# Kernel tuning notes

Measured on AMD Instinct MI355X. Metric: run time of the kernel, lower is better.

The kernel has to match this reference:

```python
import jax, jax.numpy as jnp
import numpy as np

DIM = 64
H = 4
POS_DIM = 4
NUM_IDS = 16
B = 2048
N = 64


def setup_inputs() -> dict:
    key = jax.random.key(0)
    ks = jax.random.split(key, 16)
    d8 = DIM // 8
    stdv = 1.0 / np.sqrt(DIM * DIM)
    inp = {
        "x": jax.random.normal(ks[0], (B, N, DIM), jnp.float32),
        "pos": jax.random.normal(ks[1], (B, N, POS_DIM), jnp.float32),
        "strength": jax.random.normal(ks[2], (512,), jnp.float32),
        "embed_id1": 3,
        # weights stored [in, out] (torch Linear weight transposed)
        "Wq": jax.random.normal(ks[3], (DIM, DIM), jnp.float32) * 0.05,
        "Wk": jax.random.normal(ks[4], (DIM, DIM), jnp.float32) * 0.05,
        "pos_W1": jax.random.normal(ks[5], (POS_DIM, POS_DIM), jnp.float32) * 0.3,
        "pos_b1": jnp.zeros((POS_DIM,), jnp.float32),
        "pos_W2": jax.random.normal(ks[6], (POS_DIM, d8), jnp.float32) * 0.3,
        "pos_b2": jnp.zeros((d8,), jnp.float32),
        "head_W": jax.random.normal(ks[7], (d8, H), jnp.float32) * 0.3,
        "head_b": jnp.zeros((H,), jnp.float32),
        "gate": jnp.ones((H,), jnp.float32),
        "embeds": jax.random.uniform(ks[8], (NUM_IDS, DIM * DIM), jnp.float32, -stdv, stdv),
        "out_W": jax.random.normal(ks[9], (DIM, DIM), jnp.float32) * 0.05,
        "out_b": jnp.zeros((DIM,), jnp.float32),
        "str_W": jax.random.normal(ks[10], (512, 64), jnp.float32) * 0.04,
        "str_b": jnp.zeros((64,), jnp.float32),
    }
    return inp


def reference(x, pos, strength, embed_id1, Wq, Wk, pos_W1, pos_b1, pos_W2, pos_b2,
              head_W, head_b, gate, embeds, out_W, out_b, str_W, str_b):
    Bb, Nn, dim = x.shape
    h = gate.shape[0]
    dh = dim // h

    # strength projection, added to dynamic-weight V
    s64 = strength @ str_W + str_b                       # [dim]
    E = embeds[embed_id1].reshape(dim, dim)              # per-sample V weight
    v = x @ E.T + s64                                    # F.linear(x, E) + strength
    v = v.reshape(Bb, Nn, h, dh).transpose(0, 2, 1, 3)   # [B,H,N,dh]

    # QK attention
    q = (x @ Wq).reshape(Bb, Nn, h, dh).transpose(0, 2, 1, 3)
    k = (x @ Wk).reshape(Bb, Nn, h, dh).transpose(0, 2, 1, 3)
    attn = jax.nn.softmax(jnp.einsum('bhqd,bhkd->bhqk', q, k) / np.sqrt(dh), axis=-1)

    # pairwise relative-position attention
    p = jax.nn.relu(pos @ pos_W1 + pos_b1) @ pos_W2 + pos_b2          # [B,N,dim//8]
    diff = p[:, :, None, :] - p[:, None, :, :]                        # [B,N,N,dim//8]
    pos_logits = jnp.einsum('bqkf,fh->bhqk', diff, head_W) + head_b[None, :, None, None]
    pos_attn = jax.nn.softmax(pos_logits, axis=-1)

    # sigmoid-gated mixing + renormalization
    g = jax.nn.sigmoid(gate)[None, :, None, None]
    attn = (1.0 - g) * attn + g * pos_attn
    attn = attn / jnp.sum(attn, axis=-1, keepdims=True)

    out = jnp.einsum('bhqk,bhkd->bhqd', attn, v)
    out = out.transpose(0, 2, 1, 3).reshape(Bb, Nn, dim)
    return out @ out_W + out_b
```

## Files before the change

kernel.cpp:

```cpp
#include <hip/hip_runtime.h>

typedef unsigned short u16;
typedef unsigned int u32;
typedef short bf8 __attribute__((ext_vector_type(8)));
typedef float f4v __attribute__((ext_vector_type(4)));
typedef float f16v __attribute__((ext_vector_type(16)));

#define STR 72

__device__ __forceinline__ u32 f2bf(float f){
    union{float f;u32 i;}c; c.f=f; u32 i=c.i;
    return (i + 0x7FFFu + ((i>>16)&1u)) >> 16;
}

__device__ __forceinline__ void stage_row16(const float* __restrict__ g, short* __restrict__ dst,
                                            int n, int c0){
    const float4* p = (const float4*)(g + n*64 + c0);
    float4 a=p[0], b=p[1], c=p[2], d=p[3];
    uint4 o0, o1;
    o0.x = f2bf(a.x)|(f2bf(a.y)<<16); o0.y = f2bf(a.z)|(f2bf(a.w)<<16);
    o0.z = f2bf(b.x)|(f2bf(b.y)<<16); o0.w = f2bf(b.z)|(f2bf(b.w)<<16);
    o1.x = f2bf(c.x)|(f2bf(c.y)<<16); o1.y = f2bf(c.z)|(f2bf(c.w)<<16);
    o1.z = f2bf(d.x)|(f2bf(d.y)<<16); o1.w = f2bf(d.z)|(f2bf(d.w)<<16);
    *(uint4*)&dst[n*STR + c0]     = o0;
    *(uint4*)&dst[n*STR + c0 + 8] = o1;
}

__device__ __forceinline__ void copy8k(const u16* __restrict__ src, short* __restrict__ dst, int t){
    const int r = t >> 2, cs = (t & 3) << 4;
    const uint4* s = (const uint4*)(src + r*64 + cs);
    uint4 a = s[0], b = s[1];
    *(uint4*)&dst[r*STR + cs]     = a;
    *(uint4*)&dst[r*STR + cs + 8] = b;
}

__device__ __forceinline__ void mmlin(const short* __restrict__ X, const short* __restrict__ Wt,
                                      int w, int l15, int quad, f4v c[4]){
    bf8 a0 = *(const bf8*)&X[(16*w + l15)*STR + quad*8];
    bf8 a1 = *(const bf8*)&X[(16*w + l15)*STR + 32 + quad*8];
    #pragma unroll
    for (int nt=0; nt<4; ++nt){
        bf8 b0 = *(const bf8*)&Wt[(16*nt + l15)*STR + quad*8];
        bf8 b1 = *(const bf8*)&Wt[(16*nt + l15)*STR + 32 + quad*8];
        c[nt] = __builtin_amdgcn_mfma_f32_16x16x32_bf16(a0, b0, c[nt], 0,0,0);
        c[nt] = __builtin_amdgcn_mfma_f32_16x16x32_bf16(a1, b1, c[nt], 0,0,0);
    }
}

__global__ __launch_bounds__(256) void pre_kernel(
    const float* __restrict__ pos, const float* __restrict__ strength,
    const int* __restrict__ embed_id,
    const float* __restrict__ Wq, const float* __restrict__ Wk,
    const float* __restrict__ pW1, const float* __restrict__ pb1,
    const float* __restrict__ pW2, const float* __restrict__ pb2,
    const float* __restrict__ hW, const float* __restrict__ embeds,
    const float* __restrict__ oW, const float* __restrict__ sW,
    const float* __restrict__ sb,
    float* __restrict__ ws_s64, float* __restrict__ ws_pat,
    u16* __restrict__ ws_wq, u16* __restrict__ ws_wk,
    u16* __restrict__ ws_ow, u16* __restrict__ ws_e, int B)
{
    const int blk = blockIdx.x;
    const int t = threadIdx.x;

    if (blk < B) {
        __shared__ float t_l[4][64];
        if (t < 64) {
            float pv[4], h1[4], p8[8];
            const float* gp = pos + ((size_t)blk*64 + t)*4;
            #pragma unroll
            for (int i = 0; i < 4; ++i) pv[i] = gp[i];
            #pragma unroll
            for (int j = 0; j < 4; ++j){
                float a = pb1[j];
                #pragma unroll
                for (int i = 0; i < 4; ++i) a = fmaf(pv[i], pW1[i*4+j], a);
                h1[j] = fmaxf(a, 0.f);
            }
            #pragma unroll
            for (int f = 0; f < 8; ++f){
                float a = pb2[f];
                #pragma unroll
                for (int j = 0; j < 4; ++j) a = fmaf(h1[j], pW2[j*8+f], a);
                p8[f] = a;
            }
            #pragma unroll
            for (int h = 0; h < 4; ++h){
                float a = 0.f;
                #pragma unroll
                for (int f = 0; f < 8; ++f) a = fmaf(p8[f], hW[f*4+h], a);
                t_l[h][t] = a;
            }
        }
        __syncthreads();
        const int h = t >> 6, k = t & 63;
        float v0 = -t_l[h][k];
        float m = v0;
        #pragma unroll
        for (int off = 32; off; off >>= 1) m = fmaxf(m, __shfl_xor(m, off));
        float e = __expf(v0 - m);
        float ssum = e;
        #pragma unroll
        for (int off = 32; off; off >>= 1) ssum += __shfl_xor(ssum, off);
        ws_pat[((size_t)blk*4 + h)*64 + k] = e / ssum;
        return;
    }

    const int j = blk - B;
    if (j < 3) {
        const float* W = (j==0) ? Wq : (j==1) ? Wk : oW;
        u16* dst = (j==0) ? ws_wq : (j==1) ? ws_wk : ws_ow;
        const int kp = t >> 3, ng = t & 7;
        const float4* r0 = (const float4*)(W + (2*kp  )*64 + 8*ng);
        const float4* r1 = (const float4*)(W + (2*kp+1)*64 + 8*ng);
        float4 a0=r0[0], a1=r0[1], b0=r1[0], b1=r1[1];
        float lo[8]={a0.x,a0.y,a0.z,a0.w,a1.x,a1.y,a1.z,a1.w};
        float hi[8]={b0.x,b0.y,b0.z,b0.w,b1.x,b1.y,b1.z,b1.w};
        #pragma unroll
        for (int i=0;i<8;++i)
            *(u32*)&dst[(8*ng+i)*64 + 2*kp] = f2bf(lo[i]) | (f2bf(hi[i])<<16);
    } else {
        __shared__ float sp[4][64];
        {
            const int n = t >> 2, c0 = (t & 3) << 4;
            const float4* p = (const float4*)(embeds + (size_t)(*embed_id)*4096 + n*64 + c0);
            float4 a=p[0], b=p[1], c=p[2], d=p[3];
            uint4 o0, o1;
            o0.x = f2bf(a.x)|(f2bf(a.y)<<16); o0.y = f2bf(a.z)|(f2bf(a.w)<<16);
            o0.z = f2bf(b.x)|(f2bf(b.y)<<16); o0.w = f2bf(b.z)|(f2bf(b.w)<<16);
            o1.x = f2bf(c.x)|(f2bf(c.y)<<16); o1.y = f2bf(c.z)|(f2bf(c.w)<<16);
            o1.z = f2bf(d.x)|(f2bf(d.y)<<16); o1.w = f2bf(d.z)|(f2bf(d.w)<<16);
            *(uint4*)&ws_e[n*64 + c0]     = o0;
            *(uint4*)&ws_e[n*64 + c0 + 8] = o1;
        }
        {
            const int d = t & 63, part = t >> 6;
            const float* wp = sW + part*128*64 + d;
            const float* s  = strength + part*128;
            float acc = 0.f;
            #pragma unroll 8
            for (int i = 0; i < 128; ++i) acc = fmaf(s[i], wp[i*64], acc);
            sp[part][d] = acc;
        }
        __syncthreads();
        if (t < 64) ws_s64[t] = sp[0][t] + sp[1][t] + sp[2][t] + sp[3][t] + sb[t];
    }
}

__global__ __launch_bounds__(256, 2) void attn_main_kernel(
    const float* __restrict__ x, const float* __restrict__ gate, const float* __restrict__ ob,
    const float* __restrict__ ws_s64, const float* __restrict__ ws_pat,
    const u16* __restrict__ ws_wq, const u16* __restrict__ ws_wk,
    const u16* __restrict__ ws_ow, const u16* __restrict__ ws_e,
    float* __restrict__ out)
{
    __shared__ short B0[64*STR];
    __shared__ short B1[64*STR];
    __shared__ short B2[64*STR];
    __shared__ short B3[64*STR];
    __shared__ short VT[64*STR];
    __shared__ short PX[64*STR];

    const int t    = threadIdx.x;
    const int b    = blockIdx.x;
    const int lane = t & 63;
    const int w    = t >> 6;
    const int l15  = lane & 15;
    const int l31  = lane & 31;
    const int l5   = lane >> 5;
    const int quad = lane >> 4;
    const int n    = t >> 2;
    const int c0   = (t & 3) << 4;

    stage_row16(x + (size_t)b*4096, B0, n, c0);
    copy8k(ws_wq, B1, t);
    copy8k(ws_wk, VT, t);

    uint4 eA, eB, owA, owB;
    {
        const int r = t >> 2, cs = (t & 3) << 4;
        const uint4* se = (const uint4*)(ws_e + r*64 + cs);
        eA = se[0]; eB = se[1];
        const uint4* so = (const uint4*)(ws_ow + r*64 + cs);
        owA = so[0]; owB = so[1];
    }
    float svv[4];
    #pragma unroll
    for (int nt=0;nt<4;++nt) svv[nt] = ws_s64[16*nt + l15];
    float g = 1.f/(1.f + __expf(-gate[w]));
    float obv[4];
    #pragma unroll
    for (int nt=0;nt<4;++nt) obv[nt] = ob[16*nt + l15];
    __syncthreads();

    {
        f4v cq[4], ck[4];
        #pragma unroll
        for (int nt=0;nt<4;++nt){
            cq[nt][0]=0.f;cq[nt][1]=0.f;cq[nt][2]=0.f;cq[nt][3]=0.f;
            ck[nt][0]=0.f;ck[nt][1]=0.f;ck[nt][2]=0.f;ck[nt][3]=0.f;
        }
        mmlin(B0, B1, w, l15, quad, cq);
        mmlin(B0, VT, w, l15, quad, ck);
        __syncthreads();
        #pragma unroll
        for (int nt=0;nt<4;++nt)
            #pragma unroll
            for (int r=0;r<4;++r){
                B2[(16*w + quad*4 + r)*STR + 16*nt + l15] = (short)f2bf(0.25f*cq[nt][r]);
                B3[(16*w + quad*4 + r)*STR + 16*nt + l15] = (short)f2bf(ck[nt][r]);
            }
        const int r = t >> 2, cs = (t & 3) << 4;
        *(uint4*)&B1[r*STR + cs]     = eA;
        *(uint4*)&B1[r*STR + cs + 8] = eB;
    }
    __syncthreads();

    {
        f4v c[4];
        #pragma unroll
        for (int nt=0;nt<4;++nt){ c[nt][0]=0.f;c[nt][1]=0.f;c[nt][2]=0.f;c[nt][3]=0.f; }
        mmlin(B0, B1, w, l15, quad, c);
        __syncthreads();
        #pragma unroll
        for (int nt=0;nt<4;++nt){
            float sv = svv[nt];
            uint2 pk;
            pk.x = f2bf(c[nt][0]+sv) | (f2bf(c[nt][1]+sv)<<16);
            pk.y = f2bf(c[nt][2]+sv) | (f2bf(c[nt][3]+sv)<<16);
            *(uint2*)&VT[(16*nt + l15)*STR + 16*w + quad*4] = pk;
        }
        const int r = t >> 2, cs = (t & 3) << 4;
        *(uint4*)&B1[r*STR + cs]     = owA;
        *(uint4*)&B1[r*STR + cs + 8] = owB;
    }
    __syncthreads();

    f16v S[2][2];
    {
        bf8 ka0 = *(const bf8*)&B3[(     l31)*STR + 16*w + 8*l5];
        bf8 ka1 = *(const bf8*)&B3[(32 + l31)*STR + 16*w + 8*l5];
        bf8 qb0 = *(const bf8*)&B2[(     l31)*STR + 16*w + 8*l5];
        bf8 qb1 = *(const bf8*)&B2[(32 + l31)*STR + 16*w + 8*l5];
        #pragma unroll
        for (int mt=0;mt<2;++mt)
            #pragma unroll
            for (int nt=0;nt<2;++nt)
                #pragma unroll
                for (int i=0;i<16;++i) S[mt][nt][i] = 0.f;
        S[0][0] = __builtin_amdgcn_mfma_f32_32x32x16_bf16(ka0, qb0, S[0][0], 0,0,0);
        S[0][1] = __builtin_amdgcn_mfma_f32_32x32x16_bf16(ka0, qb1, S[0][1], 0,0,0);
        S[1][0] = __builtin_amdgcn_mfma_f32_32x32x16_bf16(ka1, qb0, S[1][0], 0,0,0);
        S[1][1] = __builtin_amdgcn_mfma_f32_32x32x16_bf16(ka1, qb1, S[1][1], 0,0,0);
    }
    float ep[32];
    {
        const float* pp = ws_pat + ((size_t)b*4 + w)*64;
        #pragma unroll
        for (int mt=0;mt<2;++mt)
            #pragma unroll
            for (int rg=0;rg<4;++rg){
                float4 tv = *(const float4*)&pp[32*mt + 8*rg + 4*l5];
                ep[mt*16+rg*4+0] = g*tv.x; ep[mt*16+rg*4+1] = g*tv.y;
                ep[mt*16+rg*4+2] = g*tv.z; ep[mt*16+rg*4+3] = g*tv.w;
            }
    }
    float inv[2];
    #pragma unroll
    for (int nt=0;nt<2;++nt){
        float m = S[0][nt][0];
        #pragma unroll
        for (int i=1;i<16;++i) m = fmaxf(m, S[0][nt][i]);
        #pragma unroll
        for (int i=0;i<16;++i) m = fmaxf(m, S[1][nt][i]);
        m = fmaxf(m, __shfl_xor(m, 32));
        float l = 0.f;
        #pragma unroll
        for (int mt=0;mt<2;++mt)
            #pragma unroll
            for (int i=0;i<16;++i){ float e = __expf(S[mt][nt][i]-m); S[mt][nt][i] = e; l += e; }
        l += __shfl_xor(l, 32);
        float c1 = (1.f - g) / l;
        float tot = 0.f;
        #pragma unroll
        for (int mt=0;mt<2;++mt)
            #pragma unroll
            for (int i=0;i<16;++i){ float a = fmaf(c1, S[mt][nt][i], ep[mt*16+i]); S[mt][nt][i] = a; tot += a; }
        tot += __shfl_xor(tot, 32);
        inv[nt] = 1.f / tot;
    }
    __syncthreads();

    short* Pb = (w==0) ? B0 : (w==1) ? PX : (w==2) ? B2 : B3;
    #pragma unroll
    for (int nt=0;nt<2;++nt)
        #pragma unroll
        for (int mt=0;mt<2;++mt)
            #pragma unroll
            for (int rg=0;rg<4;++rg){
                float v0 = S[mt][nt][rg*4+0]*inv[nt], v1 = S[mt][nt][rg*4+1]*inv[nt];
                float v2 = S[mt][nt][rg*4+2]*inv[nt], v3 = S[mt][nt][rg*4+3]*inv[nt];
                uint2 pk;
                pk.x = f2bf(v0) | (f2bf(v1)<<16);
                pk.y = f2bf(v2) | (f2bf(v3)<<16);
                *(uint2*)&Pb[(32*nt + l31)*STR + 32*mt + 8*rg + 4*l5] = pk;
            }

    f4v o[4];
    {
        bf8 bv0 = *(const bf8*)&VT[(16*w + l15)*STR + quad*8];
        bf8 bv1 = *(const bf8*)&VT[(16*w + l15)*STR + 32 + quad*8];
        #pragma unroll
        for (int mt=0;mt<4;++mt){
            o[mt][0]=0.f;o[mt][1]=0.f;o[mt][2]=0.f;o[mt][3]=0.f;
            bf8 a0 = *(const bf8*)&Pb[(16*mt + l15)*STR + quad*8];
            bf8 a1 = *(const bf8*)&Pb[(16*mt + l15)*STR + 32 + quad*8];
            o[mt] = __builtin_amdgcn_mfma_f32_16x16x32_bf16(a0, bv0, o[mt], 0,0,0);
            o[mt] = __builtin_amdgcn_mfma_f32_16x16x32_bf16(a1, bv1, o[mt], 0,0,0);
        }
    }
    __syncthreads();

    #pragma unroll
    for (int mt=0;mt<4;++mt)
        #pragma unroll
        for (int r=0;r<4;++r)
            B3[(16*mt + quad*4 + r)*STR + 16*w + l15] = (short)f2bf(o[mt][r]);
    __syncthreads();

    {
        f4v c[4];
        #pragma unroll
        for (int nt=0;nt<4;++nt){
            c[nt][0]=obv[nt];c[nt][1]=obv[nt];c[nt][2]=obv[nt];c[nt][3]=obv[nt];
        }
        mmlin(B3, B1, w, l15, quad, c);
        #pragma unroll
        for (int nt=0;nt<4;++nt)
            #pragma unroll
            for (int r=0;r<4;++r)
                out[((size_t)b*64 + 16*w + quad*4 + r)*64 + 16*nt + l15] = c[nt][r];
    }
}

extern "C" void kernel_launch(void* const* d_in, const int* in_sizes, int n_in,
                              void* d_out, int out_size, void* d_ws, size_t ws_size,
                              hipStream_t stream) {
    const int B = in_sizes[0] / (64 * 64);

    float* ws_s64 = (float*)d_ws;
    float* ws_pat = ws_s64 + 64;
    u16*   ws_wq  = (u16*)(ws_pat + (size_t)B*4*64);
    u16*   ws_wk  = ws_wq + 4096;
    u16*   ws_ow  = ws_wk + 4096;
    u16*   ws_e   = ws_ow + 4096;

    pre_kernel<<<B + 4, 256, 0, stream>>>(
        (const float*)d_in[1],  (const float*)d_in[2],  (const int*)d_in[3],
        (const float*)d_in[4],  (const float*)d_in[5],
        (const float*)d_in[6],  (const float*)d_in[7],  (const float*)d_in[8],  (const float*)d_in[9],
        (const float*)d_in[10], (const float*)d_in[13], (const float*)d_in[14],
        (const float*)d_in[16], (const float*)d_in[17],
        ws_s64, ws_pat, ws_wq, ws_wk, ws_ow, ws_e, B);

    attn_main_kernel<<<B, 256, 0, stream>>>(
        (const float*)d_in[0],  (const float*)d_in[12], (const float*)d_in[15],
        ws_s64, ws_pat, ws_wq, ws_wk, ws_ow, ws_e,
        (float*)d_out);
}
```

Baseline: 143.3 us.

## Fuse positional attention into main kernel and read weights directly from global

The per-batch positional MLP and softmax move out of the pre-kernel and into the main attention kernel. Each wave now computes its own head's positional attention into a small LDS array, so the pre-kernel shrinks to 4 blocks and the ws_pat workspace round trip is gone. The Wq, Wk, E and out_W MFMA B operands are read straight from the global bf16 workspace instead of being staged in LDS, which removes several copies and block-wide barriers. The freed LDS allows the launch bound to rise to 3 blocks per CU, at the cost of repeated global/L2 weight reads in every block and redundant MLP work per wave.

New measurement: 153.5 us. 7.1% more time.

```diff
diff --git a/kernel.cpp b/kernel.cpp
--- a/kernel.cpp
+++ b/kernel.cpp
@@ -26,87 +26,28 @@
     *(uint4*)&dst[n*STR + c0 + 8] = o1;
 }
 
-__device__ __forceinline__ void copy8k(const u16* __restrict__ src, short* __restrict__ dst, int t){
-    const int r = t >> 2, cs = (t & 3) << 4;
-    const uint4* s = (const uint4*)(src + r*64 + cs);
-    uint4 a = s[0], b = s[1];
-    *(uint4*)&dst[r*STR + cs]     = a;
-    *(uint4*)&dst[r*STR + cs + 8] = b;
-}
-
-__device__ __forceinline__ void mmlin(const short* __restrict__ X, const short* __restrict__ Wt,
-                                      int w, int l15, int quad, f4v c[4]){
-    bf8 a0 = *(const bf8*)&X[(16*w + l15)*STR + quad*8];
-    bf8 a1 = *(const bf8*)&X[(16*w + l15)*STR + 32 + quad*8];
+__device__ __forceinline__ void mmgB(const u16* __restrict__ Wt, bf8 a0, bf8 a1,
+                                     int l15, int quad, f4v c[4]){
     #pragma unroll
     for (int nt=0; nt<4; ++nt){
-        bf8 b0 = *(const bf8*)&Wt[(16*nt + l15)*STR + quad*8];
-        bf8 b1 = *(const bf8*)&Wt[(16*nt + l15)*STR + 32 + quad*8];
+        bf8 b0 = *(const bf8*)&Wt[(16*nt + l15)*64 + quad*8];
+        bf8 b1 = *(const bf8*)&Wt[(16*nt + l15)*64 + 32 + quad*8];
         c[nt] = __builtin_amdgcn_mfma_f32_16x16x32_bf16(a0, b0, c[nt], 0,0,0);
         c[nt] = __builtin_amdgcn_mfma_f32_16x16x32_bf16(a1, b1, c[nt], 0,0,0);
     }
 }
 
 __global__ __launch_bounds__(256) void pre_kernel(
-    const float* __restrict__ pos, const float* __restrict__ strength,
     const int* __restrict__ embed_id,
-    const float* __restrict__ Wq, const float* __restrict__ Wk,
-    const float* __restrict__ pW1, const float* __restrict__ pb1,
-    const float* __restrict__ pW2, const float* __restrict__ pb2,
-    const float* __restrict__ hW, const float* __restrict__ embeds,
-    const float* __restrict__ oW, const float* __restrict__ sW,
-    const float* __restrict__ sb,
-    float* __restrict__ ws_s64, float* __restrict__ ws_pat,
-    u16* __restrict__ ws_wq, u16* __restrict__ ws_wk,
-    u16* __restrict__ ws_ow, u16* __restrict__ ws_e, int B)
+    const float* __restrict__ Wq, const float* __restrict__ Wk, const float* __restrict__ oW,
+    const float* __restrict__ embeds, const float* __restrict__ sW, const float* __restrict__ sb,
+    const float* __restrict__ strength,
+    float* __restrict__ ws_s64, u16* __restrict__ ws_wq, u16* __restrict__ ws_wk,
+    u16* __restrict__ ws_ow, u16* __restrict__ ws_e)
 {
-    const int blk = blockIdx.x;
+    const int j = blockIdx.x;
     const int t = threadIdx.x;
 
-    if (blk < B) {
-        __shared__ float t_l[4][64];
-        if (t < 64) {
-            float pv[4], h1[4], p8[8];
-            const float* gp = pos + ((size_t)blk*64 + t)*4;
-            #pragma unroll
-            for (int i = 0; i < 4; ++i) pv[i] = gp[i];
-            #pragma unroll
-            for (int j = 0; j < 4; ++j){
-                float a = pb1[j];
-                #pragma unroll
-                for (int i = 0; i < 4; ++i) a = fmaf(pv[i], pW1[i*4+j], a);
-                h1[j] = fmaxf(a, 0.f);
-            }
-            #pragma unroll
-            for (int f = 0; f < 8; ++f){
-                float a = pb2[f];
-                #pragma unroll
-                for (int j = 0; j < 4; ++j) a = fmaf(h1[j], pW2[j*8+f], a);
-                p8[f] = a;
-            }
-            #pragma unroll
-            for (int h = 0; h < 4; ++h){
-                float a = 0.f;
-                #pragma unroll
-                for (int f = 0; f < 8; ++f) a = fmaf(p8[f], hW[f*4+h], a);
-                t_l[h][t] = a;
-            }
-        }
-        __syncthreads();
-        const int h = t >> 6, k = t & 63;
-        float v0 = -t_l[h][k];
-        float m = v0;
-        #pragma unroll
-        for (int off = 32; off; off >>= 1) m = fmaxf(m, __shfl_xor(m, off));
-        float e = __expf(v0 - m);
-        float ssum = e;
-        #pragma unroll
-        for (int off = 32; off; off >>= 1) ssum += __shfl_xor(ssum, off);
-        ws_pat[((size_t)blk*4 + h)*64 + k] = e / ssum;
-        return;
-    }
-
-    const int j = blk - B;
     if (j < 3) {
         const float* W = (j==0) ? Wq : (j==1) ? Wk : oW;
         u16* dst = (j==0) ? ws_wq : (j==1) ? ws_wk : ws_ow;
@@ -147,9 +88,13 @@
     }
 }
 
-__global__ __launch_bounds__(256, 2) void attn_main_kernel(
-    const float* __restrict__ x, const float* __restrict__ gate, const float* __restrict__ ob,
-    const float* __restrict__ ws_s64, const float* __restrict__ ws_pat,
+__global__ __launch_bounds__(256, 3) void attn_main_kernel(
+    const float* __restrict__ x, const float* __restrict__ pos,
+    const float* __restrict__ gate, const float* __restrict__ ob,
+    const float* __restrict__ pW1, const float* __restrict__ pb1,
+    const float* __restrict__ pW2, const float* __restrict__ pb2,
+    const float* __restrict__ hW,
+    const float* __restrict__ ws_s64,
     const u16* __restrict__ ws_wq, const u16* __restrict__ ws_wk,
     const u16* __restrict__ ws_ow, const u16* __restrict__ ws_e,
     float* __restrict__ out)
@@ -159,7 +104,7 @@
     __shared__ short B2[64*STR];
     __shared__ short B3[64*STR];
     __shared__ short VT[64*STR];
-    __shared__ short PX[64*STR];
+    __shared__ float pat_l[4][64];
 
     const int t    = threadIdx.x;
     const int b    = blockIdx.x;
@@ -173,36 +118,63 @@
     const int c0   = (t & 3) << 4;
 
     stage_row16(x + (size_t)b*4096, B0, n, c0);
-    copy8k(ws_wq, B1, t);
-    copy8k(ws_wk, VT, t);
-
-    uint4 eA, eB, owA, owB;
-    {
-        const int r = t >> 2, cs = (t & 3) << 4;
-        const uint4* se = (const uint4*)(ws_e + r*64 + cs);
-        eA = se[0]; eB = se[1];
-        const uint4* so = (const uint4*)(ws_ow + r*64 + cs);
-        owA = so[0]; owB = so[1];
-    }
+
+    float g = 1.f/(1.f + __expf(-gate[w]));
+    {
+        const float4 pv = *(const float4*)(pos + ((size_t)b*64 + lane)*4);
+        float h1[4], p8[8];
+        #pragma unroll
+        for (int jj = 0; jj < 4; ++jj){
+            float a = pb1[jj];
+            a = fmaf(pv.x, pW1[0*4+jj], a);
+            a = fmaf(pv.y, pW1[1*4+jj], a);
+            a = fmaf(pv.z, pW1[2*4+jj], a);
+            a = fmaf(pv.w, pW1[3*4+jj], a);
+            h1[jj] = fmaxf(a, 0.f);
+        }
+        #pragma unroll
+        for (int f = 0; f < 8; ++f){
+            float a = pb2[f];
+            #pragma unroll
+            for (int jj = 0; jj < 4; ++jj) a = fmaf(h1[jj], pW2[jj*8+f], a);
+            p8[f] = a;
+        }
+        float tv = 0.f;
+        #pragma unroll
+        for (int f = 0; f < 8; ++f) tv = fmaf(p8[f], hW[f*4+w], tv);
+        float v0 = -tv;
+        float m = v0;
+        #pragma unroll
+        for (int off = 32; off; off >>= 1) m = fmaxf(m, __shfl_xor(m, off));
+        float e = __expf(v0 - m);
+        float ssum = e;
+        #pragma unroll
+        for (int off = 32; off; off >>= 1) ssum += __shfl_xor(ssum, off);
+        pat_l[w][lane] = g * (e / ssum);
+    }
+
     float svv[4];
     #pragma unroll
     for (int nt=0;nt<4;++nt) svv[nt] = ws_s64[16*nt + l15];
-    float g = 1.f/(1.f + __expf(-gate[w]));
     float obv[4];
     #pragma unroll
     for (int nt=0;nt<4;++nt) obv[nt] = ob[16*nt + l15];
-    __syncthreads();
-
-    {
-        f4v cq[4], ck[4];
+
+    asm volatile("" ::: "memory");
+
+    {
+        bf8 xa0 = *(const bf8*)&B0[(16*w + l15)*STR + quad*8];
+        bf8 xa1 = *(const bf8*)&B0[(16*w + l15)*STR + 32 + quad*8];
+        f4v cq[4], ck[4], cv[4];
         #pragma unroll
         for (int nt=0;nt<4;++nt){
             cq[nt][0]=0.f;cq[nt][1]=0.f;cq[nt][2]=0.f;cq[nt][3]=0.f;
             ck[nt][0]=0.f;ck[nt][1]=0.f;ck[nt][2]=0.f;ck[nt][3]=0.f;
-        }
-        mmlin(B0, B1, w, l15, quad, cq);
-        mmlin(B0, VT, w, l15, quad, ck);
-        __syncthreads();
+            cv[nt][0]=0.f;cv[nt][1]=0.f;cv[nt][2]=0.f;cv[nt][3]=0.f;
+        }
+        mmgB(ws_wq, xa0, xa1, l15, quad, cq);
+        mmgB(ws_wk, xa0, xa1, l15, quad, ck);
+        mmgB(ws_e,  xa0, xa1, l15, quad, cv);
         #pragma unroll
         for (int nt=0;nt<4;++nt)
             #pragma unroll
@@ -210,29 +182,14 @@
                 B2[(16*w + quad*4 + r)*STR + 16*nt + l15] = (short)f2bf(0.25f*cq[nt][r]);
                 B3[(16*w + quad*4 + r)*STR + 16*nt + l15] = (short)f2bf(ck[nt][r]);
             }
-        const int r = t >> 2, cs = (t & 3) << 4;
-        *(uint4*)&B1[r*STR + cs]     = eA;
-        *(uint4*)&B1[r*STR + cs + 8] = eB;
-    }
-    __syncthreads();
-
-    {
-        f4v c[4];
-        #pragma unroll
-        for (int nt=0;nt<4;++nt){ c[nt][0]=0.f;c[nt][1]=0.f;c[nt][2]=0.f;c[nt][3]=0.f; }
-        mmlin(B0, B1, w, l15, quad, c);
-        __syncthreads();
         #pragma unroll
         for (int nt=0;nt<4;++nt){
             float sv = svv[nt];
             uint2 pk;
-            pk.x = f2bf(c[nt][0]+sv) | (f2bf(c[nt][1]+sv)<<16);
-            pk.y = f2bf(c[nt][2]+sv) | (f2bf(c[nt][3]+sv)<<16);
+            pk.x = f2bf(cv[nt][0]+sv) | (f2bf(cv[nt][1]+sv)<<16);
+            pk.y = f2bf(cv[nt][2]+sv) | (f2bf(cv[nt][3]+sv)<<16);
             *(uint2*)&VT[(16*nt + l15)*STR + 16*w + quad*4] = pk;
         }
-        const int r = t >> 2, cs = (t & 3) << 4;
-        *(uint4*)&B1[r*STR + cs]     = owA;
-        *(uint4*)&B1[r*STR + cs + 8] = owB;
     }
     __syncthreads();
 
@@ -253,19 +210,7 @@
         S[1][0] = __builtin_amdgcn_mfma_f32_32x32x16_bf16(ka1, qb0, S[1][0], 0,0,0);
         S[1][1] = __builtin_amdgcn_mfma_f32_32x32x16_bf16(ka1, qb1, S[1][1], 0,0,0);
     }
-    float ep[32];
-    {
-        const float* pp = ws_pat + ((size_t)b*4 + w)*64;
-        #pragma unroll
-        for (int mt=0;mt<2;++mt)
-            #pragma unroll
-            for (int rg=0;rg<4;++rg){
-                float4 tv = *(const float4*)&pp[32*mt + 8*rg + 4*l5];
-                ep[mt*16+rg*4+0] = g*tv.x; ep[mt*16+rg*4+1] = g*tv.y;
-                ep[mt*16+rg*4+2] = g*tv.z; ep[mt*16+rg*4+3] = g*tv.w;
-            }
-    }
-    float inv[2];
+    float inv_[2];
     #pragma unroll
     for (int nt=0;nt<2;++nt){
         float m = S[0][nt][0];
@@ -285,26 +230,36 @@
         #pragma unroll
         for (int mt=0;mt<2;++mt)
             #pragma unroll
-            for (int i=0;i<16;++i){ float a = fmaf(c1, S[mt][nt][i], ep[mt*16+i]); S[mt][nt][i] = a; tot += a; }
+            for (int rg=0;rg<4;++rg){
+                const float4 tv = *(const float4*)&pat_l[w][32*mt + 8*rg + 4*l5];
+                float a0 = fmaf(c1, S[mt][nt][rg*4+0], tv.x);
+                float a1 = fmaf(c1, S[mt][nt][rg*4+1], tv.y);
+                float a2 = fmaf(c1, S[mt][nt][rg*4+2], tv.z);
+                float a3 = fmaf(c1, S[mt][nt][rg*4+3], tv.w);
+                S[mt][nt][rg*4+0]=a0; S[mt][nt][rg*4+1]=a1;
+                S[mt][nt][rg*4+2]=a2; S[mt][nt][rg*4+3]=a3;
+                tot += a0+a1+a2+a3;
+            }
         tot += __shfl_xor(tot, 32);
-        inv[nt] = 1.f / tot;
+        inv_[nt] = 1.f / tot;
     }
     __syncthreads();
 
-    short* Pb = (w==0) ? B0 : (w==1) ? PX : (w==2) ? B2 : B3;
+    short* Pb = (w==0) ? B0 : (w==1) ? B1 : (w==2) ? B2 : B3;
     #pragma unroll
     for (int nt=0;nt<2;++nt)
         #pragma unroll
         for (int mt=0;mt<2;++mt)
             #pragma unroll
             for (int rg=0;rg<4;++rg){
-                float v0 = S[mt][nt][rg*4+0]*inv[nt], v1 = S[mt][nt][rg*4+1]*inv[nt];
-                float v2 = S[mt][nt][rg*4+2]*inv[nt], v3 = S[mt][nt][rg*4+3]*inv[nt];
+                float v0 = S[mt][nt][rg*4+0]*inv_[nt], v1 = S[mt][nt][rg*4+1]*inv_[nt];
+                float v2 = S[mt][nt][rg*4+2]*inv_[nt], v3 = S[mt][nt][rg*4+3]*inv_[nt];
                 uint2 pk;
                 pk.x = f2bf(v0) | (f2bf(v1)<<16);
                 pk.y = f2bf(v2) | (f2bf(v3)<<16);
                 *(uint2*)&Pb[(32*nt + l31)*STR + 32*mt + 8*rg + 4*l5] = pk;
             }
+    asm volatile("" ::: "memory");
 
     f4v o[4];
     {
@@ -329,12 +284,14 @@
     __syncthreads();
 
     {
+        bf8 ca0 = *(const bf8*)&B3[(16*w + l15)*STR + quad*8];
+        bf8 ca1 = *(const bf8*)&B3[(16*w + l15)*STR + 32 + quad*8];
         f4v c[4];
         #pragma unroll
         for (int nt=0;nt<4;++nt){
             c[nt][0]=obv[nt];c[nt][1]=obv[nt];c[nt][2]=obv[nt];c[nt][3]=obv[nt];
         }
-        mmlin(B3, B1, w, l15, quad, c);
+        mmgB(ws_ow, ca0, ca1, l15, quad, c);
         #pragma unroll
         for (int nt=0;nt<4;++nt)
             #pragma unroll
@@ -349,22 +306,23 @@
     const int B = in_sizes[0] / (64 * 64);
 
     float* ws_s64 = (float*)d_ws;
-    float* ws_pat = ws_s64 + 64;
-    u16*   ws_wq  = (u16*)(ws_pat + (size_t)B*4*64);
+    u16*   ws_wq  = (u16*)(ws_s64 + 64);
     u16*   ws_wk  = ws_wq + 4096;
     u16*   ws_ow  = ws_wk + 4096;
     u16*   ws_e   = ws_ow + 4096;
 
-    pre_kernel<<<B + 4, 256, 0, stream>>>(
-        (const float*)d_in[1],  (const float*)d_in[2],  (const int*)d_in[3],
-        (const float*)d_in[4],  (const float*)d_in[5],
+    pre_kernel<<<4, 256, 0, stream>>>(
+        (const int*)d_in[3],
+        (const float*)d_in[4],  (const float*)d_in[5],  (const float*)d_in[14],
+        (const float*)d_in[13], (const float*)d_in[16], (const float*)d_in[17],
+        (const float*)d_in[2],
+        ws_s64, ws_wq, ws_wk, ws_ow, ws_e);
+
+    attn_main_kernel<<<B, 256, 0, stream>>>(
+        (const float*)d_in[0],  (const float*)d_in[1],
+        (const float*)d_in[12], (const float*)d_in[15],
         (const float*)d_in[6],  (const float*)d_in[7],  (const float*)d_in[8],  (const float*)d_in[9],
-        (const float*)d_in[10], (const float*)d_in[13], (const float*)d_in[14],
-        (const float*)d_in[16], (const float*)d_in[17],
-        ws_s64, ws_pat, ws_wq, ws_wk, ws_ow, ws_e, B);
-
-    attn_main_kernel<<<B, 256, 0, stream>>>(
-        (const float*)d_in[0],  (const float*)d_in[12], (const float*)d_in[15],
-        ws_s64, ws_pat, ws_wq, ws_wk, ws_ow, ws_e,
+        (const float*)d_in[10],
+        ws_s64, ws_wq, ws_wk, ws_ow, ws_e,
         (float*)d_out);
 }
```
